# Kernel optimization log

Measured on AMD Instinct MI355X. Metric: run time of the kernel, lower is better.

The kernel has to match this reference:

```python
import jax, jax.numpy as jnp
import numpy as np

N, E = 50000, 800000
IN_DIM, HIDDEN, OUT_DIM, LAYERS = 128, 64, 40, 3


def setup_inputs() -> dict:
    key = jax.random.key(0)
    ks = jax.random.split(key, 12)
    glorot = lambda k, fi, fo: jax.random.normal(k, (fi, fo), jnp.float32) * np.sqrt(2.0 / (fi + fo)).astype(np.float32)
    return {
        "x": jax.random.normal(ks[0], (N, IN_DIM), jnp.float32),
        "edge_index": jax.random.randint(ks[1], (2, E), 0, N, jnp.int64),
        "edge_weight": jax.random.uniform(ks[2], (E,), jnp.float32),
        "W1": glorot(ks[3], IN_DIM, HIDDEN), "b1": jnp.zeros((HIDDEN,), jnp.float32),
        "W2": glorot(ks[4], HIDDEN, HIDDEN), "b2": jnp.zeros((HIDDEN,), jnp.float32),
        "W3": glorot(ks[5], HIDDEN, HIDDEN), "b3": jnp.zeros((HIDDEN,), jnp.float32),
        "Wlin": glorot(ks[6], HIDDEN * LAYERS, OUT_DIM), "blin": jnp.zeros((OUT_DIM,), jnp.float32),
    }


def reference(x, edge_index, edge_weight, W1, b1, W2, b2, W3, b3, Wlin, blin):
    src, dst = edge_index[0], edge_index[1]

    def gcn_conv(h, W, b):
        # GCNConv with normalize=False: linear transform, then weighted sum aggregation at dst, then bias.
        h = h @ W                                   # [N, hidden]
        msg = h[src] * edge_weight[:, None]          # [E, hidden] gather + scale
        agg = jax.ops.segment_sum(msg, dst, num_segments=h.shape[0])  # scatter-add
        return agg + b

    outs = []
    h = x
    for W, b in ((W1, b1), (W2, b2), (W3, b3)):
        h = jax.nn.relu(gcn_conv(h, W, b))           # dropout is identity at inference
        outs.append(h)

    hjk = jnp.concatenate(outs, axis=-1)             # JumpingKnowledge mode='cat' -> [N, hidden*layers]
    return hjk @ Wlin + blin                         # [N, out_dim]
```

## Files before the change

kernel.cpp:

```cpp
#include <hip/hip_runtime.h>

#define HID 64
#define JK_DIM 192
#define OUT_DIM 40
#define AP 136
#define HP 72
#define W_PITCH 196
#define FG_PITCH 44

typedef __attribute__((ext_vector_type(8))) short bf16x8;
typedef __attribute__((ext_vector_type(4))) float f32x4;

__device__ inline unsigned short f2b(float f) {
    unsigned u = __float_as_uint(f);
    unsigned r = u + 0x7FFF + ((u >> 16) & 1);
    return (unsigned short)(r >> 16);
}
__device__ inline float b2f(unsigned short u) {
    return __uint_as_float(((unsigned)u) << 16);
}
__device__ inline float blo(unsigned u) { return __uint_as_float(u << 16); }
__device__ inline float bhi(unsigned u) { return __uint_as_float(u & 0xFFFF0000u); }
__device__ inline unsigned pack2(float a, float b) {
    return (unsigned)f2b(a) | ((unsigned)f2b(b) << 16);
}

__global__ __launch_bounds__(256) void prep(int* __restrict__ deg, int n,
                                            const float* __restrict__ W,
                                            float* __restrict__ Wt,
                                            int* __restrict__ gctr) {
    int i = blockIdx.x * 256 + threadIdx.x;
    if (i == 0) gctr[0] = 0;
    if (i < n) deg[i] = 0;
    if (i < JK_DIM * OUT_DIM) {
        int k = i / OUT_DIM;
        int c = i - k * OUT_DIM;
        Wt[c * JK_DIM + k] = W[i];
    }
}

__global__ __launch_bounds__(256) void hist_dst(const int* __restrict__ dst,
                                                int* __restrict__ deg,
                                                unsigned short* __restrict__ rank,
                                                int E, int part) {
    int p = blockIdx.x & 7;
    int bid = blockIdx.x >> 3;
    int nblk = gridDim.x >> 3;
    int lo = p * part, hi = lo + part;
    int E4 = E >> 2;
    for (int q = bid * 256 + threadIdx.x; q < E4; q += nblk * 256) {
        int4 d4 = ((const int4*)dst)[q];
        int e = q * 4;
        if (d4.x >= lo && d4.x < hi) rank[e + 0] = (unsigned short)atomicAdd(&deg[d4.x], 1);
        if (d4.y >= lo && d4.y < hi) rank[e + 1] = (unsigned short)atomicAdd(&deg[d4.y], 1);
        if (d4.z >= lo && d4.z < hi) rank[e + 2] = (unsigned short)atomicAdd(&deg[d4.z], 1);
        if (d4.w >= lo && d4.w < hi) rank[e + 3] = (unsigned short)atomicAdd(&deg[d4.w], 1);
    }
    if (bid == 0 && threadIdx.x < (E & 3)) {
        int e = (E & ~3) + threadIdx.x;
        int d = dst[e];
        if (d >= lo && d < hi) rank[e] = (unsigned short)atomicAdd(&deg[d], 1);
    }
}

__global__ __launch_bounds__(256) void scan_fused(const int* __restrict__ deg,
                                                  int* __restrict__ off,
                                                  int* __restrict__ gctr, int n) {
    __shared__ int tmp[256];
    __shared__ int base;
    int i = blockIdx.x * 256 + threadIdx.x;
    int v = (i < n) ? deg[i] : 0;
    tmp[threadIdx.x] = v;
    __syncthreads();
    for (int d = 1; d < 256; d <<= 1) {
        int t = (threadIdx.x >= d) ? tmp[threadIdx.x - d] : 0;
        __syncthreads();
        tmp[threadIdx.x] += t;
        __syncthreads();
    }
    if (threadIdx.x == 255) base = atomicAdd(gctr, tmp[255]);
    __syncthreads();
    if (i < n) off[i] = base + tmp[threadIdx.x] - v;
}

__global__ __launch_bounds__(256) void fill_and_gemm(
        const int* __restrict__ src, const int* __restrict__ dst,
        const float* __restrict__ ew, const int* __restrict__ off,
        const unsigned short* __restrict__ rank,
        unsigned* __restrict__ ecsr, int E,
        const float* __restrict__ x, const float* __restrict__ W1,
        unsigned short* __restrict__ linb, int n, int nFill) {
    __shared__ unsigned short Ah[64 * AP];
    __shared__ unsigned short Wt[64 * AP];
    int tid = threadIdx.x;
    if ((int)blockIdx.x < nFill) {
        int q = blockIdx.x * 256 + tid;
        int E4 = E >> 2;
        if (q < E4) {
            int4 d4 = ((const int4*)dst)[q];
            int4 s4 = ((const int4*)src)[q];
            float4 wv = ((const float4*)ew)[q];
            ushort4 r4 = ((const ushort4*)rank)[q];
            ecsr[off[d4.x] + r4.x] = (unsigned)s4.x | ((unsigned)f2b(wv.x) << 16);
            ecsr[off[d4.y] + r4.y] = (unsigned)s4.y | ((unsigned)f2b(wv.y) << 16);
            ecsr[off[d4.z] + r4.z] = (unsigned)s4.z | ((unsigned)f2b(wv.z) << 16);
            ecsr[off[d4.w] + r4.w] = (unsigned)s4.w | ((unsigned)f2b(wv.w) << 16);
        }
        if (blockIdx.x == 0 && tid < (E & 3)) {
            int e = (E & ~3) + tid;
            int d = dst[e];
            ecsr[off[d] + rank[e]] = (unsigned)src[e] | ((unsigned)f2b(ew[e]) << 16);
        }
        return;
    }
    int row0 = (blockIdx.x - nFill) * 64;
    if (row0 >= n) return;
    for (int i = tid; i < 64 * 32; i += 256) {
        int r = i >> 5;
        int c4 = (i & 31) * 4;
        int grow = row0 + r;
        if (grow >= n) grow = n - 1;
        float4 v = *(const float4*)(x + (long)grow * 128 + c4);
        ushort4 o;
        o.x = f2b(v.x); o.y = f2b(v.y); o.z = f2b(v.z); o.w = f2b(v.w);
        *(ushort4*)(Ah + r * AP + c4) = o;
    }
    for (int i = tid; i < 128 * 16; i += 256) {
        int k = i >> 4;
        int n4 = (i & 15) * 4;
        float4 v = *(const float4*)(W1 + (long)k * 64 + n4);
        Wt[(n4 + 0) * AP + k] = f2b(v.x);
        Wt[(n4 + 1) * AP + k] = f2b(v.y);
        Wt[(n4 + 2) * AP + k] = f2b(v.z);
        Wt[(n4 + 3) * AP + k] = f2b(v.w);
    }
    __syncthreads();

    int wave = tid >> 6;
    int lane = tid & 63;
    int lr = lane & 15;
    int lk = (lane >> 4) * 8;
    f32x4 acc[4];
#pragma unroll
    for (int nf = 0; nf < 4; ++nf) acc[nf] = (f32x4){0.f, 0.f, 0.f, 0.f};
#pragma unroll
    for (int k0 = 0; k0 < 128; k0 += 32) {
        bf16x8 a = *(const bf16x8*)(Ah + (wave * 16 + lr) * AP + k0 + lk);
#pragma unroll
        for (int nf = 0; nf < 4; ++nf) {
            bf16x8 b = *(const bf16x8*)(Wt + (nf * 16 + lr) * AP + k0 + lk);
            acc[nf] = __builtin_amdgcn_mfma_f32_16x16x32_bf16(a, b, acc[nf], 0, 0, 0);
        }
    }
    int mbase = wave * 16 + (lane >> 4) * 4;
#pragma unroll
    for (int nf = 0; nf < 4; ++nf) {
#pragma unroll
        for (int r = 0; r < 4; ++r) {
            int grow = row0 + mbase + r;
            if (grow < n)
                linb[(long)grow * HID + nf * 16 + lr] = f2b(acc[nf][r]);
        }
    }
}

__global__ __launch_bounds__(256) void gemm_b16in(const unsigned short* __restrict__ h,
                                                  const float* __restrict__ W,
                                                  unsigned short* __restrict__ outb,
                                                  int n) {
    __shared__ unsigned short Hs[64 * HP];
    __shared__ unsigned short Wt[64 * HP];
    int tid = threadIdx.x;
    int row0 = blockIdx.x * 64;
    if (row0 >= n) return;
    for (int i = tid; i < 64 * 8; i += 256) {
        int r = i >> 3;
        int q = (i & 7) * 8;
        int grow = row0 + r;
        if (grow >= n) grow = n - 1;
        uint4 u = *(const uint4*)(h + (long)grow * JK_DIM + q);
        *(uint4*)(Hs + r * HP + q) = u;
    }
    for (int i = tid; i < 64 * 16; i += 256) {
        int k = i >> 4;
        int n4 = (i & 15) * 4;
        float4 v = *(const float4*)(W + (long)k * 64 + n4);
        Wt[(n4 + 0) * HP + k] = f2b(v.x);
        Wt[(n4 + 1) * HP + k] = f2b(v.y);
        Wt[(n4 + 2) * HP + k] = f2b(v.z);
        Wt[(n4 + 3) * HP + k] = f2b(v.w);
    }
    __syncthreads();

    int wave = tid >> 6;
    int lane = tid & 63;
    int lr = lane & 15;
    int lk = (lane >> 4) * 8;
    f32x4 acc[4];
#pragma unroll
    for (int nf = 0; nf < 4; ++nf) acc[nf] = (f32x4){0.f, 0.f, 0.f, 0.f};
#pragma unroll
    for (int k0 = 0; k0 < 64; k0 += 32) {
        bf16x8 a = *(const bf16x8*)(Hs + (wave * 16 + lr) * HP + k0 + lk);
#pragma unroll
        for (int nf = 0; nf < 4; ++nf) {
            bf16x8 b = *(const bf16x8*)(Wt + (nf * 16 + lr) * HP + k0 + lk);
            acc[nf] = __builtin_amdgcn_mfma_f32_16x16x32_bf16(a, b, acc[nf], 0, 0, 0);
        }
    }
    int mbase = wave * 16 + (lane >> 4) * 4;
#pragma unroll
    for (int nf = 0; nf < 4; ++nf) {
#pragma unroll
        for (int r = 0; r < 4; ++r) {
            int grow = row0 + mbase + r;
            if (grow < n)
                outb[(long)grow * HID + nf * 16 + lr] = f2b(acc[nf][r]);
        }
    }
}

__global__ __launch_bounds__(256) void aggregate(const unsigned short* __restrict__ linb,
                                                 const unsigned* __restrict__ ecsr,
                                                 const int* __restrict__ off,
                                                 const int* __restrict__ deg,
                                                 const float* __restrict__ bias,
                                                 unsigned short* __restrict__ hout, int n) {
    int cl = threadIdx.x & 7;
    float4 bLo = *(const float4*)(bias + cl * 8);
    float4 bHi = *(const float4*)(bias + cl * 8 + 4);
    int grp = (blockIdx.x * 256 + threadIdx.x) >> 3;
    int ngrp = (gridDim.x * 256) >> 3;
    for (int node = grp; node < n; node += ngrp) {
        int start = off[node];
        int cnt = deg[node];
        float acc[8];
#pragma unroll
        for (int i = 0; i < 8; ++i) acc[i] = 0.f;

        int s[8];
        float w[8];
#pragma unroll
        for (int t = 0; t < 8; ++t) {
            s[t] = 0; w[t] = 0.f;
            if (t < cnt) {
                unsigned m = ecsr[start + t];
                s[t] = (int)(m & 0xFFFFu);
                w[t] = b2f((unsigned short)(m >> 16));
            }
        }
        for (int bb = 0; bb < cnt; bb += 8) {
            int s2[8];
            float w2[8];
#pragma unroll
            for (int t = 0; t < 8; ++t) {
                int e = bb + 8 + t;
                s2[t] = 0; w2[t] = 0.f;
                if (e < cnt) {
                    unsigned m = ecsr[start + e];
                    s2[t] = (int)(m & 0xFFFFu);
                    w2[t] = b2f((unsigned short)(m >> 16));
                }
            }
            uint4 u[8];
#pragma unroll
            for (int t = 0; t < 8; ++t)
                u[t] = *(const uint4*)(linb + (long)s[t] * HID + cl * 8);
#pragma unroll
            for (int t = 0; t < 8; ++t) {
                acc[0] += blo(u[t].x) * w[t];
                acc[1] += bhi(u[t].x) * w[t];
                acc[2] += blo(u[t].y) * w[t];
                acc[3] += bhi(u[t].y) * w[t];
                acc[4] += blo(u[t].z) * w[t];
                acc[5] += bhi(u[t].z) * w[t];
                acc[6] += blo(u[t].w) * w[t];
                acc[7] += bhi(u[t].w) * w[t];
            }
#pragma unroll
            for (int t = 0; t < 8; ++t) { s[t] = s2[t]; w[t] = w2[t]; }
        }

        uint4 o;
        o.x = pack2(fmaxf(acc[0] + bLo.x, 0.f), fmaxf(acc[1] + bLo.y, 0.f));
        o.y = pack2(fmaxf(acc[2] + bLo.z, 0.f), fmaxf(acc[3] + bLo.w, 0.f));
        o.z = pack2(fmaxf(acc[4] + bHi.x, 0.f), fmaxf(acc[5] + bHi.y, 0.f));
        o.w = pack2(fmaxf(acc[6] + bHi.z, 0.f), fmaxf(acc[7] + bHi.w, 0.f));
        *(uint4*)(hout + (long)node * JK_DIM + cl * 8) = o;
    }
}

__global__ __launch_bounds__(256) void final_gemm(const unsigned short* __restrict__ hcat,
                                                  const float* __restrict__ Wt,
                                                  const float* __restrict__ b,
                                                  float* __restrict__ out, int n) {
    __shared__ float pool[OUT_DIM * W_PITCH];
    int tid = threadIdx.x;
    for (int i = tid; i < OUT_DIM * 48; i += 256) {
        int c = i / 48;
        int q = (i - c * 48) * 4;
        *(float4*)(pool + c * W_PITCH + q) = *(const float4*)(Wt + (long)c * JK_DIM + q);
    }
    __syncthreads();

    int rg = tid >> 3;
    int cg = tid & 7;
    int c0 = cg * 5;
    int row0 = blockIdx.x * 64;
    int r0 = row0 + rg * 2;
    int ra = r0 < n ? r0 : n - 1;
    int rb = r0 + 1 < n ? r0 + 1 : n - 1;
    const unsigned short* ha = hcat + (long)ra * JK_DIM;
    const unsigned short* hb = hcat + (long)rb * JK_DIM;

    float acc[2][5];
#pragma unroll
    for (int r = 0; r < 2; ++r)
#pragma unroll
        for (int i = 0; i < 5; ++i) acc[r][i] = 0.f;

#pragma unroll 4
    for (int k = 0; k < JK_DIM; k += 4) {
        uint2 ua = *(const uint2*)(ha + k);
        uint2 ub = *(const uint2*)(hb + k);
        float4 va = make_float4(blo(ua.x), bhi(ua.x), blo(ua.y), bhi(ua.y));
        float4 vb = make_float4(blo(ub.x), bhi(ub.x), blo(ub.y), bhi(ub.y));
        float4 w0 = *(const float4*)(pool + (c0 + 0) * W_PITCH + k);
        float4 w1 = *(const float4*)(pool + (c0 + 1) * W_PITCH + k);
        float4 w2 = *(const float4*)(pool + (c0 + 2) * W_PITCH + k);
        float4 w3 = *(const float4*)(pool + (c0 + 3) * W_PITCH + k);
        float4 w4 = *(const float4*)(pool + (c0 + 4) * W_PITCH + k);
        acc[0][0] += va.x * w0.x + va.y * w0.y + va.z * w0.z + va.w * w0.w;
        acc[0][1] += va.x * w1.x + va.y * w1.y + va.z * w1.z + va.w * w1.w;
        acc[0][2] += va.x * w2.x + va.y * w2.y + va.z * w2.z + va.w * w2.w;
        acc[0][3] += va.x * w3.x + va.y * w3.y + va.z * w3.z + va.w * w3.w;
        acc[0][4] += va.x * w4.x + va.y * w4.y + va.z * w4.z + va.w * w4.w;
        acc[1][0] += vb.x * w0.x + vb.y * w0.y + vb.z * w0.z + vb.w * w0.w;
        acc[1][1] += vb.x * w1.x + vb.y * w1.y + vb.z * w1.z + vb.w * w1.w;
        acc[1][2] += vb.x * w2.x + vb.y * w2.y + vb.z * w2.z + vb.w * w2.w;
        acc[1][3] += vb.x * w3.x + vb.y * w3.y + vb.z * w3.z + vb.w * w3.w;
        acc[1][4] += vb.x * w4.x + vb.y * w4.y + vb.z * w4.z + vb.w * w4.w;
    }

    __syncthreads();
#pragma unroll
    for (int r = 0; r < 2; ++r)
#pragma unroll
        for (int i = 0; i < 5; ++i)
            pool[(rg * 2 + r) * FG_PITCH + c0 + i] = acc[r][i] + b[c0 + i];
    __syncthreads();

    if (row0 + 64 <= n) {
        for (int i = tid; i < 64 * OUT_DIM / 4; i += 256) {
            int f = i * 4;
            int row = f / OUT_DIM;
            int col = f - row * OUT_DIM;
            *(float4*)(out + (long)(row0 + row) * OUT_DIM + col) =
                *(const float4*)(pool + row * FG_PITCH + col);
        }
    } else {
        for (int i = tid; i < 64 * OUT_DIM; i += 256) {
            int row = i / OUT_DIM;
            int col = i - row * OUT_DIM;
            if (row0 + row < n)
                out[(long)(row0 + row) * OUT_DIM + col] = pool[row * FG_PITCH + col];
        }
    }
}

extern "C" void kernel_launch(void* const* d_in, const int* in_sizes, int n_in,
                              void* d_out, int out_size, void* d_ws, size_t ws_size,
                              hipStream_t stream) {
    const float* x    = (const float*)d_in[0];
    const int*   ei   = (const int*)d_in[1];
    const float* ew   = (const float*)d_in[2];
    const float* W1   = (const float*)d_in[3];
    const float* b1   = (const float*)d_in[4];
    const float* W2   = (const float*)d_in[5];
    const float* b2   = (const float*)d_in[6];
    const float* W3   = (const float*)d_in[7];
    const float* b3   = (const float*)d_in[8];
    const float* Wlin = (const float*)d_in[9];
    const float* blin = (const float*)d_in[10];
    float* out = (float*)d_out;

    const int N = in_sizes[0] / 128;
    const int E = in_sizes[2];
    const int* src = ei;
    const int* dst = ei + E;
    const int PART = (N + 7) / 8;

    char* wsb = (char*)d_ws;
    unsigned short* linb  = (unsigned short*)wsb;   wsb += (long)N * HID * 2;
    unsigned short* hcatb = (unsigned short*)wsb;   wsb += (long)N * JK_DIM * 2;
    int* deg    = (int*)wsb;                        wsb += (long)N * 4;
    int* off    = (int*)wsb;                        wsb += (long)N * 4;
    int* bsum   = (int*)wsb;                        wsb += 256 * 4;
    float* Wt   = (float*)wsb;                      wsb += (long)JK_DIM * OUT_DIM * 4;
    unsigned* ecsr = (unsigned*)wsb;
    unsigned short* rank = hcatb;
    int* gctr = bsum;

    dim3 blk(256);
    const int nblkN = (N + 255) / 256;
    dim3 gN(nblkN);
    dim3 gHist(8 * 104);
    const int nFill = ((E >> 2) + 255) / 256;
    const int nGemm = (N + 63) / 64;
    dim3 gFG(nFill + nGemm);
    dim3 gGemm((N + 63) / 64);
    dim3 gAgg((N + 31) / 32);
    dim3 gFin((N + 63) / 64);

    unsigned short* h1 = hcatb;
    unsigned short* h2 = hcatb + HID;
    unsigned short* h3 = hcatb + 2 * HID;

    prep<<<gN, blk, 0, stream>>>(deg, N, Wlin, Wt, gctr);
    hist_dst<<<gHist, blk, 0, stream>>>(dst, deg, rank, E, PART);
    scan_fused<<<gN, blk, 0, stream>>>(deg, off, gctr, N);

    fill_and_gemm<<<gFG, blk, 0, stream>>>(src, dst, ew, off, rank, ecsr, E,
                                           x, W1, linb, N, nFill);
    aggregate<<<gAgg, blk, 0, stream>>>(linb, ecsr, off, deg, b1, h1, N);

    gemm_b16in<<<gGemm, blk, 0, stream>>>(h1, W2, linb, N);
    aggregate<<<gAgg, blk, 0, stream>>>(linb, ecsr, off, deg, b2, h2, N);

    gemm_b16in<<<gGemm, blk, 0, stream>>>(h2, W3, linb, N);
    aggregate<<<gAgg, blk, 0, stream>>>(linb, ecsr, off, deg, b3, h3, N);

    final_gemm<<<gFin, blk, 0, stream>>>(hcatb, Wt, blin, out, N);
}
```

Measured before the change: 260.0 us.

## Fuse layers 2-3 into aggregate-then-transform kernels using linearity

Layers 2 and 3 now aggregate the previous hidden features over neighbours first, then multiply the aggregated 64-row tile by W in LDS with MFMA and apply bias and ReLU. This reordering (A·(hW) = (A·h)W) removes the separate GEMM kernel, its launch, and the round trip through the linb buffer for those two layers. The cost is that the gather now reads from the wider hcat rows (pitch 192) rather than a compact 64-wide buffer. Rounding the aggregate to bf16 before the matmul also changes numerics slightly.

Result: no change. 257.5 us (-0.9%).

```diff
diff --git a/kernel.cpp b/kernel.cpp
--- a/kernel.cpp
+++ b/kernel.cpp
@@ -164,62 +164,6 @@
     }
 }
 
-__global__ __launch_bounds__(256) void gemm_b16in(const unsigned short* __restrict__ h,
-                                                  const float* __restrict__ W,
-                                                  unsigned short* __restrict__ outb,
-                                                  int n) {
-    __shared__ unsigned short Hs[64 * HP];
-    __shared__ unsigned short Wt[64 * HP];
-    int tid = threadIdx.x;
-    int row0 = blockIdx.x * 64;
-    if (row0 >= n) return;
-    for (int i = tid; i < 64 * 8; i += 256) {
-        int r = i >> 3;
-        int q = (i & 7) * 8;
-        int grow = row0 + r;
-        if (grow >= n) grow = n - 1;
-        uint4 u = *(const uint4*)(h + (long)grow * JK_DIM + q);
-        *(uint4*)(Hs + r * HP + q) = u;
-    }
-    for (int i = tid; i < 64 * 16; i += 256) {
-        int k = i >> 4;
-        int n4 = (i & 15) * 4;
-        float4 v = *(const float4*)(W + (long)k * 64 + n4);
-        Wt[(n4 + 0) * HP + k] = f2b(v.x);
-        Wt[(n4 + 1) * HP + k] = f2b(v.y);
-        Wt[(n4 + 2) * HP + k] = f2b(v.z);
-        Wt[(n4 + 3) * HP + k] = f2b(v.w);
-    }
-    __syncthreads();
-
-    int wave = tid >> 6;
-    int lane = tid & 63;
-    int lr = lane & 15;
-    int lk = (lane >> 4) * 8;
-    f32x4 acc[4];
-#pragma unroll
-    for (int nf = 0; nf < 4; ++nf) acc[nf] = (f32x4){0.f, 0.f, 0.f, 0.f};
-#pragma unroll
-    for (int k0 = 0; k0 < 64; k0 += 32) {
-        bf16x8 a = *(const bf16x8*)(Hs + (wave * 16 + lr) * HP + k0 + lk);
-#pragma unroll
-        for (int nf = 0; nf < 4; ++nf) {
-            bf16x8 b = *(const bf16x8*)(Wt + (nf * 16 + lr) * HP + k0 + lk);
-            acc[nf] = __builtin_amdgcn_mfma_f32_16x16x32_bf16(a, b, acc[nf], 0, 0, 0);
-        }
-    }
-    int mbase = wave * 16 + (lane >> 4) * 4;
-#pragma unroll
-    for (int nf = 0; nf < 4; ++nf) {
-#pragma unroll
-        for (int r = 0; r < 4; ++r) {
-            int grow = row0 + mbase + r;
-            if (grow < n)
-                outb[(long)grow * HID + nf * 16 + lr] = f2b(acc[nf][r]);
-        }
-    }
-}
-
 __global__ __launch_bounds__(256) void aggregate(const unsigned short* __restrict__ linb,
                                                  const unsigned* __restrict__ ecsr,
                                                  const int* __restrict__ off,
@@ -287,6 +231,117 @@
         o.z = pack2(fmaxf(acc[4] + bHi.x, 0.f), fmaxf(acc[5] + bHi.y, 0.f));
         o.w = pack2(fmaxf(acc[6] + bHi.z, 0.f), fmaxf(acc[7] + bHi.w, 0.f));
         *(uint4*)(hout + (long)node * JK_DIM + cl * 8) = o;
+    }
+}
+
+__global__ __launch_bounds__(256) void agg_transform(
+        const unsigned short* __restrict__ hprev,
+        const unsigned* __restrict__ ecsr,
+        const int* __restrict__ off, const int* __restrict__ deg,
+        const float* __restrict__ W, const float* __restrict__ bias,
+        unsigned short* __restrict__ hout, int n) {
+    __shared__ unsigned short Hs[64 * HP];
+    __shared__ unsigned short Wt[64 * HP];
+    int tid = threadIdx.x;
+    int row0 = blockIdx.x * 64;
+    if (row0 >= n) return;
+    for (int i = tid; i < 64 * 16; i += 256) {
+        int k = i >> 4;
+        int n4 = (i & 15) * 4;
+        float4 v = *(const float4*)(W + (long)k * 64 + n4);
+        Wt[(n4 + 0) * HP + k] = f2b(v.x);
+        Wt[(n4 + 1) * HP + k] = f2b(v.y);
+        Wt[(n4 + 2) * HP + k] = f2b(v.z);
+        Wt[(n4 + 3) * HP + k] = f2b(v.w);
+    }
+    int cl = tid & 7;
+    int g0 = tid >> 3;
+    for (int gi = 0; gi < 2; ++gi) {
+        int lrow = g0 + gi * 32;
+        int node = row0 + lrow;
+        float acc[8];
+#pragma unroll
+        for (int i = 0; i < 8; ++i) acc[i] = 0.f;
+        if (node < n) {
+            int start = off[node];
+            int cnt = deg[node];
+            int s[8];
+            float w[8];
+#pragma unroll
+            for (int t = 0; t < 8; ++t) {
+                s[t] = 0; w[t] = 0.f;
+                if (t < cnt) {
+                    unsigned m = ecsr[start + t];
+                    s[t] = (int)(m & 0xFFFFu);
+                    w[t] = b2f((unsigned short)(m >> 16));
+                }
+            }
+            for (int bb = 0; bb < cnt; bb += 8) {
+                int s2[8];
+                float w2[8];
+#pragma unroll
+                for (int t = 0; t < 8; ++t) {
+                    int e = bb + 8 + t;
+                    s2[t] = 0; w2[t] = 0.f;
+                    if (e < cnt) {
+                        unsigned m = ecsr[start + e];
+                        s2[t] = (int)(m & 0xFFFFu);
+                        w2[t] = b2f((unsigned short)(m >> 16));
+                    }
+                }
+                uint4 u[8];
+#pragma unroll
+                for (int t = 0; t < 8; ++t)
+                    u[t] = *(const uint4*)(hprev + (long)s[t] * JK_DIM + cl * 8);
+#pragma unroll
+                for (int t = 0; t < 8; ++t) {
+                    acc[0] += blo(u[t].x) * w[t];
+                    acc[1] += bhi(u[t].x) * w[t];
+                    acc[2] += blo(u[t].y) * w[t];
+                    acc[3] += bhi(u[t].y) * w[t];
+                    acc[4] += blo(u[t].z) * w[t];
+                    acc[5] += bhi(u[t].z) * w[t];
+                    acc[6] += blo(u[t].w) * w[t];
+                    acc[7] += bhi(u[t].w) * w[t];
+                }
+#pragma unroll
+                for (int t = 0; t < 8; ++t) { s[t] = s2[t]; w[t] = w2[t]; }
+            }
+        }
+        uint4 o;
+        o.x = pack2(acc[0], acc[1]);
+        o.y = pack2(acc[2], acc[3]);
+        o.z = pack2(acc[4], acc[5]);
+        o.w = pack2(acc[6], acc[7]);
+        *(uint4*)(Hs + lrow * HP + cl * 8) = o;
+    }
+    __syncthreads();
+    int wave = tid >> 6;
+    int lane = tid & 63;
+    int lr = lane & 15;
+    int lk = (lane >> 4) * 8;
+    f32x4 d[4];
+#pragma unroll
+    for (int nf = 0; nf < 4; ++nf) d[nf] = (f32x4){0.f, 0.f, 0.f, 0.f};
+#pragma unroll
+    for (int k0 = 0; k0 < 64; k0 += 32) {
+        bf16x8 a = *(const bf16x8*)(Hs + (wave * 16 + lr) * HP + k0 + lk);
+#pragma unroll
+        for (int nf = 0; nf < 4; ++nf) {
+            bf16x8 b = *(const bf16x8*)(Wt + (nf * 16 + lr) * HP + k0 + lk);
+            d[nf] = __builtin_amdgcn_mfma_f32_16x16x32_bf16(a, b, d[nf], 0, 0, 0);
+        }
+    }
+    int mbase = wave * 16 + (lane >> 4) * 4;
+#pragma unroll
+    for (int nf = 0; nf < 4; ++nf) {
+        float bv = bias[nf * 16 + lr];
+#pragma unroll
+        for (int r = 0; r < 4; ++r) {
+            int grow = row0 + mbase + r;
+            if (grow < n)
+                hout[(long)grow * JK_DIM + nf * 16 + lr] = f2b(fmaxf(d[nf][r] + bv, 0.f));
+        }
     }
 }
 
@@ -408,7 +463,7 @@
     const int nFill = ((E >> 2) + 255) / 256;
     const int nGemm = (N + 63) / 64;
     dim3 gFG(nFill + nGemm);
-    dim3 gGemm((N + 63) / 64);
+    dim3 gTile((N + 63) / 64);
     dim3 gAgg((N + 31) / 32);
     dim3 gFin((N + 63) / 64);
 
@@ -424,11 +479,8 @@
                                            x, W1, linb, N, nFill);
     aggregate<<<gAgg, blk, 0, stream>>>(linb, ecsr, off, deg, b1, h1, N);
 
-    gemm_b16in<<<gGemm, blk, 0, stream>>>(h1, W2, linb, N);
-    aggregate<<<gAgg, blk, 0, stream>>>(linb, ecsr, off, deg, b2, h2, N);
-
-    gemm_b16in<<<gGemm, blk, 0, stream>>>(h2, W3, linb, N);
-    aggregate<<<gAgg, blk, 0, stream>>>(linb, ecsr, off, deg, b3, h3, N);
+    agg_transform<<<gTile, blk, 0, stream>>>(h1, ecsr, off, deg, W2, b2, h2, N);
+    agg_transform<<<gTile, blk, 0, stream>>>(h2, ecsr, off, deg, W3, b3, h3, N);
 
     final_gemm<<<gFin, blk, 0, stream>>>(hcatb, Wt, blin, out, N);
 }
```
